# Kernel optimization log

Hardware: AMD Instinct MI355X
Metric: run time of the kernel (lower is better)

The kernel has to match this reference:

```python
import jax, jax.numpy as jnp
import numpy as np

NUM_PERSISTENT = 16
ALIBI_ALPHA = 1.0
START_I = 0
DILATION = 1
LN_EPS = 1e-5


def setup_inputs() -> dict:
    key = jax.random.key(0)
    ks = jax.random.split(key, 16)
    B, S, C, H = 8, 1024, 512, 8
    D = C // H
    P = NUM_PERSISTENT
    Kk = 3
    x = jax.random.normal(ks[0], (B, S, C), dtype=jnp.float32)
    mask = jnp.ones((B, 1, S, S), dtype=jnp.int32)
    sc = 0.02
    Wq = jax.random.normal(ks[1], (D, D), jnp.float32) * sc
    Wk = jax.random.normal(ks[2], (D, D), jnp.float32) * sc
    Wv = jax.random.normal(ks[3], (D, D), jnp.float32) * sc
    pk = jax.random.normal(ks[4], (P, H, D), jnp.float32) * sc
    pv = jax.random.normal(ks[5], (P, H, D), jnp.float32) * sc
    th_pre = jax.random.normal(ks[6], (H, H), jnp.float32) * (1.0 / np.sqrt(H))
    th_post = jax.random.normal(ks[7], (H, H), jnp.float32) * (1.0 / np.sqrt(H))
    fc_w = jax.random.normal(ks[8], (C, C), jnp.float32) * sc
    fc_b = jnp.zeros((C,), jnp.float32)
    conv1_w = jax.random.normal(ks[9], (C, C, Kk), jnp.float32) * 0.01
    conv1_b = jnp.zeros((C,), jnp.float32)
    conv2_w = jax.random.normal(ks[10], (C, C, Kk), jnp.float32) * 0.01
    conv2_b = jnp.zeros((C,), jnp.float32)
    ln_g = jnp.ones((C,), jnp.float32)
    ln_b = jnp.zeros((C,), jnp.float32)
    return dict(x=x, mask=mask, Wq=Wq, Wk=Wk, Wv=Wv, pk=pk, pv=pv,
                th_pre=th_pre, th_post=th_post, fc_w=fc_w, fc_b=fc_b,
                conv1_w=conv1_w, conv1_b=conv1_b, conv2_w=conv2_w,
                conv2_b=conv2_b, ln_g=ln_g, ln_b=ln_b)


def _causal_conv(x_nct, w_oik, b_o, dilation):
    # padding (k-1)*d on both sides + chomp right == pad left only
    k = w_oik.shape[-1]
    p = (k - 1) * dilation
    y = jax.lax.conv_general_dilated(
        x_nct, w_oik, window_strides=(1,), padding=[(p, 0)],
        rhs_dilation=(dilation,), dimension_numbers=("NCH", "OIH", "NCH"))
    return y + b_o[None, :, None]


def reference(x, mask, Wq, Wk, Wv, pk, pv, th_pre, th_post, fc_w, fc_b,
              conv1_w, conv1_b, conv2_w, conv2_b, ln_g, ln_b):
    N, S, C = x.shape
    H = th_pre.shape[0]
    D = C // H
    P = pk.shape[0]

    # ---- MultiHeadAttention (eval: dropout = identity) ----
    xh = x.reshape(N, S, H, D)
    q = jnp.einsum("nshd,ed->nshe", xh, Wq)
    k = jnp.einsum("nshd,ed->nshe", xh, Wk)
    v = jnp.einsum("nshd,ed->nshe", xh, Wv)
    # persistent memory tokens appended along key/value length
    k = jnp.concatenate([k, jnp.broadcast_to(pk[None], (N, P, H, D))], axis=1)
    v = jnp.concatenate([v, jnp.broadcast_to(pv[None], (N, P, H, D))], axis=1)

    energy = jnp.einsum("nqhd,nkhd->nhqk", q, k)  # (N,H,S,S+P)

    # ALiBi bias (symmetric |q-k|), zero over persistent keys
    slopes = 2.0 ** (-(ALIBI_ALPHA * (jnp.arange(1, H + 1, dtype=jnp.float32) + START_I)))
    t = jnp.arange(S, dtype=jnp.float32)
    dist = jnp.abs(t[:, None] - t[None, :])  # (S,S)
    bias = -dist[None, None] * slopes[None, :, None, None]  # (1,H,S,S)
    bias = jnp.pad(bias, ((0, 0), (0, 0), (0, 0), (0, P)))
    energy = energy + bias

    # pre-softmax talking heads (1x1 conv over head axis)
    energy = jnp.einsum("hg,ngqk->nhqk", th_pre, energy)

    ext_mask = jnp.pad(mask, ((0, 0), (0, 0), (0, 0), (0, P)), constant_values=1)
    energy = jnp.where(ext_mask == 0, jnp.float32(-1e4), energy)

    attn = jax.nn.softmax(energy / jnp.sqrt(jnp.float32(C)), axis=-1)
    attn = jnp.einsum("hg,ngqk->nhqk", th_post, attn)

    att_out = jnp.einsum("nhql,nlhd->nqhd", attn, v).reshape(N, S, C)
    att_out = att_out @ fc_w.T + fc_b

    x = x + att_out  # residual (dropout1 identity in eval)

    # ---- TemporalBlock (causal dilated convs, no SE since heads>0) ----
    xc = jnp.transpose(x, (0, 2, 1))  # (N,C,S)
    h = jax.nn.relu(_causal_conv(xc, conv1_w, conv1_b, DILATION))
    h = jax.nn.relu(_causal_conv(h, conv2_w, conv2_b, DILATION))
    out = jax.nn.relu(h + xc)  # downsample is None (in==out)

    # mask out invalid frames
    conv_mask = mask[:, 0, :, 0][:, None, :]  # (N,1,S)
    out = jnp.where(conv_mask == 0, 0.0, out)

    y = jnp.transpose(out, (0, 2, 1))  # (N,S,C)
    mu = jnp.mean(y, axis=-1, keepdims=True)
    var = jnp.mean(jnp.square(y - mu), axis=-1, keepdims=True)
    y = (y - mu) * jax.lax.rsqrt(var + LN_EPS) * ln_g + ln_b
    return y
```

## Files before the change

kernel.cpp:

```cpp
#include <hip/hip_runtime.h>
#include <hip/hip_bf16.h>

#define BN 8
#define SS 1024
#define CC 512
#define HH 8
#define DD 64
#define PP 16
#define KT 1040

typedef __hip_bfloat16 bf16;
typedef unsigned char uchar;
typedef unsigned short ushort;
typedef unsigned int uint;
typedef __attribute__((ext_vector_type(8))) short short8;
typedef __attribute__((ext_vector_type(4))) float f32x4;
typedef __attribute__((ext_vector_type(2))) float f32x2;

__device__ __forceinline__ short f2s(float v){ bf16 b = __float2bfloat16(v); return *(short*)&b; }
__device__ __forceinline__ float s2f(short s){ bf16 b; *(short*)&b = s; return __bfloat162float(b); }
__device__ __forceinline__ uchar f2q(float v){
    return (uchar)__builtin_amdgcn_cvt_pk_fp8_f32(v, v, 0, false);
}

#define MFMA16(a,b,c)  __builtin_amdgcn_mfma_f32_16x16x32_bf16(a,b,c,0,0,0)
#define MFMAF8(a,b,c)  __builtin_amdgcn_mfma_f32_16x16x32_fp8_fp8(a,b,c,0,0,0)

__global__ __launch_bounds__(256) void prep_kernel(
    const float* __restrict__ fc_w, const float* __restrict__ c1w,
    const float* __restrict__ c2w, const float* __restrict__ Wq,
    const float* __restrict__ Wk, const float* __restrict__ Wv,
    const float* __restrict__ th_post,
    short* __restrict__ Bfc, uchar* __restrict__ Bc1,
    uchar* __restrict__ Bc2, short* __restrict__ Bqkv)
{
    int i = blockIdx.x*256 + threadIdx.x;
    const int NFC = 512*512, NCV = 512*1536, NQ = 3*64*64;
    if (i < NFC) {
        int c = i >> 9, r = i & 511;
        int g = r >> 6, d = r & 63;
        float s = 0.f;
        #pragma unroll
        for (int h = 0; h < 8; ++h)
            s += fc_w[(size_t)c*512 + h*64 + d] * th_post[h*8 + g];
        Bfc[i] = f2s(s);
        return;
    }
    i -= NFC;
    if (i < NCV) {
        int o = i/1536, r = i%1536, dk = r>>9, ci = r&511;
        Bc1[i] = f2q(c1w[(o*512+ci)*3+dk] * 16.f); return;
    }
    i -= NCV;
    if (i < NCV) {
        int o = i/1536, r = i%1536, dk = r>>9, ci = r&511;
        Bc2[i] = f2q(c2w[(o*512+ci)*3+dk] * 16.f); return;
    }
    i -= NCV;
    if (i < NQ) {
        int w = i >> 12, rest = i & 4095;
        const float* W = (w==0)?Wq:(w==1)?Wk:Wv;
        Bqkv[i] = f2s(W[((rest>>6)&63)*64 + (rest&63)]);
    }
}

__global__ __launch_bounds__(256) void qkv_mfma(
    const float* __restrict__ x, const short* __restrict__ Bqkv,
    uchar* __restrict__ qf, uchar* __restrict__ kf, uchar* __restrict__ vt)
{
    __shared__ short Xs[64*72];
    __shared__ short Ws[192*72];
    const int tid = threadIdx.x;
    const int m0 = blockIdx.x * 64;
    const int h = blockIdx.y;
    const int wave = tid >> 6, lane = tid & 63;
    const int lr = lane & 15, lq = lane >> 4;

    for (int i = tid; i < 1024; i += 256) {
        int r = i >> 4, cg = (i & 15)*4;
        float4 v = *(const float4*)(x + (size_t)(m0+r)*CC + h*64 + cg);
        Xs[r*72+cg+0] = f2s(v.x); Xs[r*72+cg+1] = f2s(v.y);
        Xs[r*72+cg+2] = f2s(v.z); Xs[r*72+cg+3] = f2s(v.w);
    }
    for (int i = tid; i < 3072; i += 256) {
        int r = i >> 4, cg = (i & 15)*4;
        *(short4*)(Ws + r*72 + cg) = *(const short4*)(Bqkv + (size_t)r*64 + cg);
    }
    __syncthreads();

    f32x4 acc[12];
    #pragma unroll
    for (int nt = 0; nt < 12; ++nt) acc[nt] = {0.f,0.f,0.f,0.f};
    #pragma unroll
    for (int ks = 0; ks < 2; ++ks) {
        int ko = ks*32 + lq*8;
        short8 a = *(const short8*)(Xs + (wave*16 + lr)*72 + ko);
        #pragma unroll
        for (int nt = 0; nt < 12; ++nt) {
            short8 b = *(const short8*)(Ws + (nt*16 + lr)*72 + ko);
            acc[nt] = MFMA16(a, b, acc[nt]);
        }
    }
    #pragma unroll
    for (int nt = 0; nt < 12; ++nt) {
        int ep = nt*16 + lr;
        int w = ep >> 6, e = ep & 63;
        #pragma unroll
        for (int reg = 0; reg < 4; ++reg) {
            int m = m0 + wave*16 + lq*4 + reg;
            int n = m >> 10, s = m & 1023;
            float v = acc[nt][reg];
            if (w == 0)      qf[((size_t)(n*HH+h)*SS + s)*DD + e] = f2q(v);
            else if (w == 1) kf[((size_t)(n*HH+h)*KT + s)*DD + e] = f2q(v);
            else             vt[(((size_t)(n*HH+h))*DD + e)*KT + s] = f2q(v);
        }
    }
}

__global__ __launch_bounds__(256) void persist_kernel(
    const float* __restrict__ pk, const float* __restrict__ pv,
    uchar* __restrict__ kf, uchar* __restrict__ vt)
{
    int idx = blockIdx.x*256 + threadIdx.x;
    if (idx >= BN*HH*PP*DD) return;
    int d = idx & 63, p = (idx >> 6) & 15, h = (idx >> 10) & 7, n = idx >> 13;
    size_t src = ((size_t)p*HH + h)*DD + d;
    kf[(((size_t)(n*HH+h))*KT + SS + p)*DD + d] = f2q(pk[src]);
    vt[(((size_t)(n*HH+h))*DD + d)*KT + SS + p] = f2q(pv[src]);
}

__global__ __launch_bounds__(256) void energy_mfma8(
    const uchar* __restrict__ qf, const uchar* __restrict__ kf,
    uchar* __restrict__ E)
{
    __shared__ uchar Qs[64*72];
    __shared__ uchar Ks[64*72];
    const int tid = threadIdx.x;
    const int kt = blockIdx.x;
    const int mt = blockIdx.y;
    const int nh = blockIdx.z;
    const int wave = tid >> 6, lane = tid & 63;
    const int lr = lane & 15, lq = lane >> 4;

    #pragma unroll
    for (int j = 0; j < 2; ++j) {
        int i = tid + j*256;
        int r = i >> 3, c8 = (i & 7)*8;
        *(uint2*)(Qs + r*72 + c8) =
            *(const uint2*)(qf + ((size_t)nh*SS + mt*64 + r)*DD + c8);
        int kcol = kt*64 + r;
        uint2 kv = {0u, 0u};
        if (kcol < KT)
            kv = *(const uint2*)(kf + ((size_t)nh*KT + kcol)*DD + c8);
        *(uint2*)(Ks + r*72 + c8) = kv;
    }
    __syncthreads();

    f32x4 acc[4];
    #pragma unroll
    for (int nt = 0; nt < 4; ++nt) acc[nt] = {0.f,0.f,0.f,0.f};
    #pragma unroll
    for (int ks = 0; ks < 2; ++ks) {
        int ko = ks*32 + lq*8;
        long a = *(const long*)(Qs + (wave*16 + lr)*72 + ko);
        #pragma unroll
        for (int nt = 0; nt < 4; ++nt) {
            long b = *(const long*)(Ks + (nt*16 + lr)*72 + ko);
            acc[nt] = MFMAF8(a, b, acc[nt]);
        }
    }
    const int n = nh >> 3, h = nh & 7;
    #pragma unroll
    for (int nt = 0; nt < 4; ++nt) {
        int kcol = kt*64 + nt*16 + lr;
        if (kcol >= KT) continue;
        #pragma unroll
        for (int reg = 0; reg < 4; ++reg) {
            int q = mt*64 + wave*16 + lq*4 + reg;
            E[(((size_t)(n*SS + q))*HH + h)*KT + kcol] = f2q(acc[nt][reg]);
        }
    }
}

__global__ __launch_bounds__(256) void softmax_kernel(
    uchar* __restrict__ E, const int* __restrict__ mask,
    const float* __restrict__ th_pre)
{
    __shared__ float thp[64];
    __shared__ float wred[4][8];
    const int tid = threadIdx.x;
    const int wave = tid >> 6, lane = tid & 63;
    const int blk = blockIdx.x;
    const int n = blk >> 10, q = blk & 1023;
    const float invs = 0.044194173824159216f;
    const float l2e  = 1.4426950408889634f;
    if (tid < 64) thp[tid] = th_pre[tid]*(invs*l2e);
    __syncthreads();
    uchar* Eb = E + (size_t)blk*HH*KT;

    const float sl[8] = {0.5f,0.25f,0.125f,0.0625f,
                         0.03125f,0.015625f,0.0078125f,0.00390625f};
    const int* mrow = mask + (size_t)n*SS*SS + (size_t)q*SS;

    const int k0 = tid*4;
    const int4 mk = *(const int4*)(mrow + k0);
    f32x4 dist;
    dist.x = fabsf((float)(q - k0));
    dist.y = fabsf((float)(q - k0 - 1));
    dist.z = fabsf((float)(q - k0 - 2));
    dist.w = fabsf((float)(q - k0 - 3));

    f32x4 tp[8];
    float tl[8];
    float sm[8];
    #pragma unroll
    for (int g = 0; g < 8; ++g) { sm[g] = 0.f; tl[g] = 0.f; }

    {
        f32x4 a[8];
        #pragma unroll
        for (int g = 0; g < 8; ++g) {
            uint u = *(const uint*)(Eb + g*KT + k0);
            f32x2 lo = __builtin_amdgcn_cvt_pk_f32_fp8((int)u, false);
            f32x2 hi = __builtin_amdgcn_cvt_pk_f32_fp8((int)u, true);
            f32x4 r; r.x = lo.x; r.y = lo.y; r.z = hi.x; r.w = hi.y;
            a[g] = r - dist*sl[g];
        }
        #pragma unroll
        for (int h = 0; h < 8; ++h) {
            f32x4 t = {0.f,0.f,0.f,0.f};
            #pragma unroll
            for (int g = 0; g < 8; ++g)
                t += a[g] * thp[h*8 + g];
            f32x4 e;
            e.x = (mk.x == 0) ? 0.f : exp2f(t.x);
            e.y = (mk.y == 0) ? 0.f : exp2f(t.y);
            e.z = (mk.z == 0) ? 0.f : exp2f(t.z);
            e.w = (mk.w == 0) ? 0.f : exp2f(t.w);
            tp[h] = e;
            sm[h] += e.x + e.y + e.z + e.w;
        }
    }
    if (tid < 16) {
        const int k = 1024 + tid;
        float a[8];
        #pragma unroll
        for (int g = 0; g < 8; ++g) {
            f32x2 r = __builtin_amdgcn_cvt_pk_f32_fp8((int)Eb[g*KT + k], false);
            a[g] = r.x;
        }
        #pragma unroll
        for (int h = 0; h < 8; ++h) {
            float t = 0.f;
            #pragma unroll
            for (int g = 0; g < 8; ++g) t = fmaf(thp[h*8 + g], a[g], t);
            float e = exp2f(t);
            tl[h] = e;
            sm[h] += e;
        }
    }
    #pragma unroll
    for (int g = 0; g < 8; ++g) {
        #pragma unroll
        for (int off = 32; off > 0; off >>= 1)
            sm[g] += __shfl_xor(sm[g], off);
    }
    if (lane == 0) {
        #pragma unroll
        for (int g = 0; g < 8; ++g) wred[wave][g] = sm[g];
    }
    __syncthreads();
    float lred[8];
    #pragma unroll
    for (int g = 0; g < 8; ++g)
        lred[g] = 1.0f / (wred[0][g] + wred[1][g] + wred[2][g] + wred[3][g]);

    #pragma unroll
    for (int h = 0; h < 8; ++h) {
        f32x4 e = tp[h] * lred[h];
        int p = __builtin_amdgcn_cvt_pk_fp8_f32(e.x, e.y, 0, false);
        p = __builtin_amdgcn_cvt_pk_fp8_f32(e.z, e.w, p, true);
        *(uint*)(Eb + h*KT + k0) = (uint)p;
    }
    if (tid < 16) {
        const int k = 1024 + tid;
        #pragma unroll
        for (int g = 0; g < 8; ++g)
            Eb[g*KT + k] = f2q(tl[g] * lred[g]);
    }
}

__device__ __forceinline__ void pv_loadP(const uchar* __restrict__ E,
    int n, int h, int ql0, int kt, int tid, uint2* rp)
{
    int r = tid >> 3, cg = (tid & 7)*8;
    int k = kt*64 + cg;
    uint2 v = {0u, 0u};
    if (k < KT)
        v = *(const uint2*)(E + (((size_t)(n*SS + ql0 + r))*HH + h)*KT + k);
    rp[0] = v;
}
__device__ __forceinline__ void pv_loadV(const uchar* __restrict__ vt,
    int nh, int kt, int tid, uint2* rv)
{
    #pragma unroll
    for (int j = 0; j < 2; ++j) {
        int i = tid + j*256;
        int r = i >> 3, cg = (i & 7)*8;
        int k = kt*64 + cg;
        uint2 v = {0u, 0u};
        if (k < KT)
            v = *(const uint2*)(vt + ((size_t)nh*DD + r)*KT + k);
        rv[j] = v;
    }
}

__global__ __launch_bounds__(256) void pv_mfma(
    const uchar* __restrict__ E, const uchar* __restrict__ vt,
    short* __restrict__ AO)
{
    __shared__ uchar Ps[32*72];
    __shared__ uchar Vs[64*72];
    const int tid = threadIdx.x;
    const int ql0 = blockIdx.x * 32;
    const int nh = blockIdx.y;
    const int n = nh >> 3, h = nh & 7;
    const int wave = tid >> 6, lane = tid & 63;
    const int lr = lane & 15, lq = lane >> 4;
    const int mh = wave & 1, nb = (wave >> 1)*32;

    uint2 rp[1], rv[2];
    pv_loadP(E, n, h, ql0, 0, tid, rp);
    pv_loadV(vt, nh, 0, tid, rv);

    f32x4 acc[2];
    acc[0] = {0.f,0.f,0.f,0.f}; acc[1] = {0.f,0.f,0.f,0.f};

    for (int kt = 0; kt < 17; ++kt) {
        if (kt) __syncthreads();
        {
            int r = tid >> 3, cg = (tid & 7)*8;
            *(uint2*)(Ps + r*72 + cg) = rp[0];
        }
        #pragma unroll
        for (int j = 0; j < 2; ++j) {
            int i = tid + j*256;
            *(uint2*)(Vs + (i >> 3)*72 + (i & 7)*8) = rv[j];
        }
        __syncthreads();
        if (kt + 1 < 17) {
            pv_loadP(E, n, h, ql0, kt+1, tid, rp);
            pv_loadV(vt, nh, kt+1, tid, rv);
        }
        #pragma unroll
        for (int ks = 0; ks < 2; ++ks) {
            int ko = ks*32 + lq*8;
            long a = *(const long*)(Ps + (mh*16 + lr)*72 + ko);
            #pragma unroll
            for (int nt = 0; nt < 2; ++nt) {
                long b = *(const long*)(Vs + (nb + nt*16 + lr)*72 + ko);
                acc[nt] = MFMAF8(a, b, acc[nt]);
            }
        }
    }
    #pragma unroll
    for (int nt = 0; nt < 2; ++nt) {
        int d = nb + nt*16 + lr;
        #pragma unroll
        for (int reg = 0; reg < 4; ++reg) {
            int qg = ql0 + mh*16 + lq*4 + reg;
            AO[((size_t)(n*SS) + qg)*CC + h*64 + d] = f2s(acc[nt][reg]);
        }
    }
}

__device__ __forceinline__ void g_load4(const short* __restrict__ src,
    size_t rowstride, int row0, int col0, int tid, short4* r)
{
    #pragma unroll
    for (int j = 0; j < 4; ++j) {
        int i = tid + j*256;
        int rr = i >> 4, cg = (i & 15)*4;
        r[j] = *(const short4*)(src + (size_t)(row0 + rr)*rowstride + col0 + cg);
    }
}
__device__ __forceinline__ void lds_store4(short* __restrict__ dst,
    int tid, const short4* r)
{
    #pragma unroll
    for (int j = 0; j < 4; ++j) {
        int i = tid + j*256;
        *(short4*)(dst + (i >> 4)*72 + (i & 15)*4) = r[j];
    }
}

__global__ __launch_bounds__(256) void fc_mfma(
    const short* __restrict__ A, const short* __restrict__ Bt,
    const float* __restrict__ bias, const float* __restrict__ x,
    short* __restrict__ out, uchar* __restrict__ out8)
{
    __shared__ short As[64*72];
    __shared__ short Bs[64*72];
    const int tid = threadIdx.x;
    const int lin = blockIdx.x + 8*blockIdx.y;
    const int xcd = lin & 7, slot = lin >> 3;
    const int m0 = (xcd*16 + (slot & 15))*64;
    const int n0 = (slot >> 4)*64;
    const int wave = tid >> 6, lane = tid & 63;
    const int lr = lane & 15, lq = lane >> 4;

    short4 ra[4], rb[4];
    g_load4(A, CC, m0, 0, tid, ra);
    g_load4(Bt, CC, n0, 0, tid, rb);

    f32x4 acc[4];
    #pragma unroll
    for (int nt = 0; nt < 4; ++nt) acc[nt] = {0.f,0.f,0.f,0.f};

    for (int kt = 0; kt < CC; kt += 64) {
        if (kt) __syncthreads();
        lds_store4(As, tid, ra);
        lds_store4(Bs, tid, rb);
        __syncthreads();
        if (kt + 64 < CC) {
            g_load4(A, CC, m0, kt+64, tid, ra);
            g_load4(Bt, CC, n0, kt+64, tid, rb);
        }
        #pragma unroll
        for (int ks = 0; ks < 2; ++ks) {
            int ko = ks*32 + lq*8;
            short8 a = *(const short8*)(As + (wave*16 + lr)*72 + ko);
            #pragma unroll
            for (int nt = 0; nt < 4; ++nt) {
                short8 b = *(const short8*)(Bs + (nt*16 + lr)*72 + ko);
                acc[nt] = MFMA16(a, b, acc[nt]);
            }
        }
    }
    #pragma unroll
    for (int nt = 0; nt < 4; ++nt) {
        int nn = n0 + nt*16 + lr;
        #pragma unroll
        for (int reg = 0; reg < 4; ++reg) {
            int m = m0 + wave*16 + lq*4 + reg;
            float v = acc[nt][reg] + bias[nn] + x[(size_t)m*CC + nn];
            out[(size_t)m*CC + nn]  = f2s(v);
            out8[(size_t)m*CC + nn] = f2q(v);
        }
    }
}

__device__ __forceinline__ void conv_loadA8(const uchar* __restrict__ A,
    int m0, int kt, int tid, uint2* ra)
{
    const int shift = (kt >> 9) - 2;
    const int ci0 = kt & 511;
    #pragma unroll
    for (int j = 0; j < 2; ++j) {
        int i = tid + j*256;
        int rr = i >> 3, c8 = (i & 7)*8;
        int m = m0 + rr;
        int s = m & (SS-1);
        uint2 v = {0u, 0u};
        if (s + shift >= 0)
            v = *(const uint2*)(A + (size_t)(m + shift)*CC + ci0 + c8);
        ra[j] = v;
    }
}
__device__ __forceinline__ void g_load8(const uchar* __restrict__ src,
    size_t rowstride, int row0, int col0, int tid, uint2* r)
{
    #pragma unroll
    for (int j = 0; j < 2; ++j) {
        int i = tid + j*256;
        int rr = i >> 3, c8 = (i & 7)*8;
        r[j] = *(const uint2*)(src + (size_t)(row0 + rr)*rowstride + col0 + c8);
    }
}
__device__ __forceinline__ void lds_store8(uchar* __restrict__ dst,
    int tid, const uint2* r)
{
    #pragma unroll
    for (int j = 0; j < 2; ++j) {
        int i = tid + j*256;
        *(uint2*)(dst + (i >> 3)*72 + (i & 7)*8) = r[j];
    }
}

__global__ __launch_bounds__(256) void conv_mfma8(
    const uchar* __restrict__ A, const uchar* __restrict__ Bt,
    const float* __restrict__ bias, uchar* __restrict__ out8,
    short* __restrict__ out16, int f8out)
{
    __shared__ uchar As[64*72];
    __shared__ uchar Bs[64*72];
    const int tid = threadIdx.x;
    const int lin = blockIdx.x + 8*blockIdx.y;
    const int xcd = lin & 7, slot = lin >> 3;
    const int m0 = (xcd*16 + (slot & 15))*64;
    const int n0 = (slot >> 4)*64;
    const int wave = tid >> 6, lane = tid & 63;
    const int lr = lane & 15, lq = lane >> 4;

    uint2 ra[2], rb[2];
    conv_loadA8(A, m0, 0, tid, ra);
    g_load8(Bt, 1536, n0, 0, tid, rb);

    f32x4 acc[4];
    #pragma unroll
    for (int nt = 0; nt < 4; ++nt) acc[nt] = {0.f,0.f,0.f,0.f};

    for (int kt = 0; kt < 1536; kt += 64) {
        if (kt) __syncthreads();
        lds_store8(As, tid, ra);
        lds_store8(Bs, tid, rb);
        __syncthreads();
        if (kt + 64 < 1536) {
            conv_loadA8(A, m0, kt+64, tid, ra);
            g_load8(Bt, 1536, n0, kt+64, tid, rb);
        }
        #pragma unroll
        for (int ks = 0; ks < 2; ++ks) {
            int ko = ks*32 + lq*8;
            long a = *(const long*)(As + (wave*16 + lr)*72 + ko);
            #pragma unroll
            for (int nt = 0; nt < 4; ++nt) {
                long b = *(const long*)(Bs + (nt*16 + lr)*72 + ko);
                acc[nt] = MFMAF8(a, b, acc[nt]);
            }
        }
    }
    #pragma unroll
    for (int nt = 0; nt < 4; ++nt) {
        int nn = n0 + nt*16 + lr;
        #pragma unroll
        for (int reg = 0; reg < 4; ++reg) {
            int m = m0 + wave*16 + lq*4 + reg;
            float v = fmaxf(acc[nt][reg]*0.0625f + bias[nn], 0.f);
            if (f8out) out8[(size_t)m*CC + nn]  = f2q(v);
            else       out16[(size_t)m*CC + nn] = f2s(v);
        }
    }
}

__global__ __launch_bounds__(256) void final_kernel(
    const short* __restrict__ c2, const short* __restrict__ xres,
    const int* __restrict__ mask, const float* __restrict__ g,
    const float* __restrict__ b, float* __restrict__ out)
{
    __shared__ float red[256];
    const int tid = threadIdx.x;
    const int m = blockIdx.x;
    const int n = m >> 10, s = m & 1023;
    const int mk = mask[(size_t)n*SS*SS + (size_t)s*SS];
    const int c0 = tid*2;

    short2 ca = *(const short2*)(c2 + (size_t)m*CC + c0);
    short2 xa = *(const short2*)(xres + (size_t)m*CC + c0);
    float v0 = fmaxf(s2f(ca.x) + s2f(xa.x), 0.f);
    float v1 = fmaxf(s2f(ca.y) + s2f(xa.y), 0.f);
    if (mk == 0) { v0 = 0.f; v1 = 0.f; }

    red[tid] = v0 + v1;
    __syncthreads();
    for (int off = 128; off > 0; off >>= 1) {
        if (tid < off) red[tid] += red[tid + off];
        __syncthreads();
    }
    float mu = red[0] * (1.0f/512.0f);
    __syncthreads();
    float d0 = v0 - mu, d1 = v1 - mu;
    red[tid] = d0*d0 + d1*d1;
    __syncthreads();
    for (int off = 128; off > 0; off >>= 1) {
        if (tid < off) red[tid] += red[tid + off];
        __syncthreads();
    }
    float rstd = rsqrtf(red[0] * (1.0f/512.0f) + 1e-5f);
    float2 gg = *(const float2*)(g + c0);
    float2 bb = *(const float2*)(b + c0);
    float2 o;
    o.x = d0*rstd*gg.x + bb.x;
    o.y = d1*rstd*gg.y + bb.y;
    *(float2*)(out + (size_t)m*CC + c0) = o;
}

extern "C" void kernel_launch(void* const* d_in, const int* in_sizes, int n_in,
                              void* d_out, int out_size, void* d_ws, size_t ws_size,
                              hipStream_t stream)
{
    const float* x      = (const float*)d_in[0];
    const int*   mask   = (const int*)  d_in[1];
    const float* Wq     = (const float*)d_in[2];
    const float* Wk     = (const float*)d_in[3];
    const float* Wv     = (const float*)d_in[4];
    const float* pk     = (const float*)d_in[5];
    const float* pv     = (const float*)d_in[6];
    const float* th_pre = (const float*)d_in[7];
    const float* th_post= (const float*)d_in[8];
    const float* fc_w   = (const float*)d_in[9];
    const float* fc_b   = (const float*)d_in[10];
    const float* c1w    = (const float*)d_in[11];
    const float* c1b    = (const float*)d_in[12];
    const float* c2w    = (const float*)d_in[13];
    const float* c2b    = (const float*)d_in[14];
    const float* lng    = (const float*)d_in[15];
    const float* lnb    = (const float*)d_in[16];
    float* out = (float*)d_out;
    (void)in_sizes; (void)n_in; (void)out_size; (void)ws_size;

    char* ws = (char*)d_ws;
    const size_t SZ_Q  = (size_t)BN*HH*SS*DD;
    const size_t SZ_K  = (size_t)BN*HH*KT*DD;
    const size_t SZ_VT = (size_t)BN*HH*DD*KT;
    const size_t SZ_E  = (size_t)BN*SS*HH*KT;
    const size_t SZ_A  = (size_t)BN*SS*CC*2;
    const size_t SZ_A8 = (size_t)BN*SS*CC;

    uchar* qf  = (uchar*)(ws);
    uchar* kf  = (uchar*)(ws + SZ_Q);
    uchar* vt  = (uchar*)(ws + SZ_Q + SZ_K);
    uchar* E   = (uchar*)(ws + SZ_Q + SZ_K + SZ_VT);
    short* AO  = (short*)(ws + SZ_Q + SZ_K + SZ_VT + SZ_E);
    char*  wend = ws + SZ_Q + SZ_K + SZ_VT + SZ_E + SZ_A;
    short* Bfc = (short*)(wend);
    uchar* Bc1 = (uchar*)(wend + 512*512*2);
    uchar* Bc2 = (uchar*)(wend + 512*512*2 + 512*1536);
    short* Bqkv= (short*)(wend + 512*512*2 + 2*512*1536);
    uchar* xres8 = (uchar*)(wend + 512*512*2 + 2*512*1536 + 3*64*64*2);
    short* c2buf = (short*)(wend + 512*512*2 + 2*512*1536 + 3*64*64*2 + SZ_A8);
    short* xres = (short*)(ws);
    uchar* h18  = (uchar*)E;

    {
        int total = 512*512 + 2*512*1536 + 3*64*64;
        prep_kernel<<<(total + 255)/256, 256, 0, stream>>>(
            fc_w, c1w, c2w, Wq, Wk, Wv, th_post, Bfc, Bc1, Bc2, Bqkv);
    }
    qkv_mfma<<<dim3(BN*SS/64, HH), 256, 0, stream>>>(x, Bqkv, qf, kf, vt);
    persist_kernel<<<(BN*HH*PP*DD + 255)/256, 256, 0, stream>>>(pk, pv, kf, vt);

    energy_mfma8<<<dim3(17, SS/64, BN*HH), 256, 0, stream>>>(qf, kf, E);
    softmax_kernel<<<BN*SS, 256, 0, stream>>>(E, mask, th_pre);
    pv_mfma<<<dim3(SS/32, BN*HH), 256, 0, stream>>>(E, vt, AO);

    fc_mfma<<<dim3(8, 128), 256, 0, stream>>>(AO, Bfc, fc_b, x, xres, xres8);
    conv_mfma8<<<dim3(8, 128), 256, 0, stream>>>(xres8, Bc1, c1b, h18, (short*)nullptr, 1);
    conv_mfma8<<<dim3(8, 128), 256, 0, stream>>>(h18, Bc2, c2b, (uchar*)nullptr, c2buf, 0);
    final_kernel<<<BN*SS, 256, 0, stream>>>(c2buf, xres, mask, lng, lnb, out);
}
```

Before: 309.1 us.

## Loop energy kernel over K tiles with register prefetch; fold ALiBi into softmax

The energy kernel now keeps each Q tile in shared memory and loops over all 17 K tiles inside one block. The next K tile is prefetched into registers while the current tile is being computed, and the grid shrinks from 17x16x64 to 16x64 blocks. The softmax kernel folds the ALiBi distance term through the head-mixing matrix into one per-head coefficient, which removes 8 multiplies per element, and masking is skipped when no element in the group is dead. Fewer blocks lower occupancy and parallelism, and the per-tile loop adds syncthreads overhead.

```diff
diff --git a/kernel.cpp b/kernel.cpp
--- a/kernel.cpp
+++ b/kernel.cpp
@@ -129,6 +129,21 @@
     vt[(((size_t)(n*HH+h))*DD + d)*KT + SS + p] = f2q(pv[src]);
 }
 
+__device__ __forceinline__ void en_loadK(const uchar* __restrict__ kf,
+    int nh, int kt, int tid, uint2* rk)
+{
+    #pragma unroll
+    for (int j = 0; j < 2; ++j) {
+        int i = tid + j*256;
+        int r = i >> 3, c8 = (i & 7)*8;
+        int kcol = kt*64 + r;
+        uint2 v = {0u, 0u};
+        if (kcol < KT)
+            v = *(const uint2*)(kf + ((size_t)nh*KT + kcol)*DD + c8);
+        rk[j] = v;
+    }
+}
+
 __global__ __launch_bounds__(256) void energy_mfma8(
     const uchar* __restrict__ qf, const uchar* __restrict__ kf,
     uchar* __restrict__ E)
@@ -136,11 +151,11 @@
     __shared__ uchar Qs[64*72];
     __shared__ uchar Ks[64*72];
     const int tid = threadIdx.x;
-    const int kt = blockIdx.x;
-    const int mt = blockIdx.y;
-    const int nh = blockIdx.z;
+    const int mt = blockIdx.x;
+    const int nh = blockIdx.y;
     const int wave = tid >> 6, lane = tid & 63;
     const int lr = lane & 15, lq = lane >> 4;
+    const int n = nh >> 3, h = nh & 7;
 
     #pragma unroll
     for (int j = 0; j < 2; ++j) {
@@ -148,36 +163,43 @@
         int r = i >> 3, c8 = (i & 7)*8;
         *(uint2*)(Qs + r*72 + c8) =
             *(const uint2*)(qf + ((size_t)nh*SS + mt*64 + r)*DD + c8);
-        int kcol = kt*64 + r;
-        uint2 kv = {0u, 0u};
-        if (kcol < KT)
-            kv = *(const uint2*)(kf + ((size_t)nh*KT + kcol)*DD + c8);
-        *(uint2*)(Ks + r*72 + c8) = kv;
-    }
-    __syncthreads();
-
-    f32x4 acc[4];
-    #pragma unroll
-    for (int nt = 0; nt < 4; ++nt) acc[nt] = {0.f,0.f,0.f,0.f};
-    #pragma unroll
-    for (int ks = 0; ks < 2; ++ks) {
-        int ko = ks*32 + lq*8;
-        long a = *(const long*)(Qs + (wave*16 + lr)*72 + ko);
+    }
+
+    uint2 rk[2];
+    en_loadK(kf, nh, 0, tid, rk);
+
+    for (int kt = 0; kt < 17; ++kt) {
+        if (kt) __syncthreads();
+        #pragma unroll
+        for (int j = 0; j < 2; ++j) {
+            int i = tid + j*256;
+            *(uint2*)(Ks + (i >> 3)*72 + (i & 7)*8) = rk[j];
+        }
+        __syncthreads();
+        if (kt + 1 < 17) en_loadK(kf, nh, kt+1, tid, rk);
+
+        f32x4 acc[4];
+        #pragma unroll
+        for (int nt = 0; nt < 4; ++nt) acc[nt] = {0.f,0.f,0.f,0.f};
+        #pragma unroll
+        for (int ks = 0; ks < 2; ++ks) {
+            int ko = ks*32 + lq*8;
+            long a = *(const long*)(Qs + (wave*16 + lr)*72 + ko);
+            #pragma unroll
+            for (int nt = 0; nt < 4; ++nt) {
+                long b = *(const long*)(Ks + (nt*16 + lr)*72 + ko);
+                acc[nt] = MFMAF8(a, b, acc[nt]);
+            }
+        }
         #pragma unroll
         for (int nt = 0; nt < 4; ++nt) {
-            long b = *(const long*)(Ks + (nt*16 + lr)*72 + ko);
-            acc[nt] = MFMAF8(a, b, acc[nt]);
-        }
-    }
-    const int n = nh >> 3, h = nh & 7;
-    #pragma unroll
-    for (int nt = 0; nt < 4; ++nt) {
-        int kcol = kt*64 + nt*16 + lr;
-        if (kcol >= KT) continue;
-        #pragma unroll
-        for (int reg = 0; reg < 4; ++reg) {
-            int q = mt*64 + wave*16 + lq*4 + reg;
-            E[(((size_t)(n*SS + q))*HH + h)*KT + kcol] = f2q(acc[nt][reg]);
+            int kcol = kt*64 + nt*16 + lr;
+            if (kcol >= KT) continue;
+            #pragma unroll
+            for (int reg = 0; reg < 4; ++reg) {
+                int q = mt*64 + wave*16 + lq*4 + reg;
+                E[(((size_t)(n*SS + q))*HH + h)*KT + kcol] = f2q(acc[nt][reg]);
+            }
         }
     }
 }
@@ -187,6 +209,7 @@
     const float* __restrict__ th_pre)
 {
     __shared__ float thp[64];
+    __shared__ float ch[8];
     __shared__ float wred[4][8];
     const int tid = threadIdx.x;
     const int wave = tid >> 6, lane = tid & 63;
@@ -195,15 +218,21 @@
     const float invs = 0.044194173824159216f;
     const float l2e  = 1.4426950408889634f;
     if (tid < 64) thp[tid] = th_pre[tid]*(invs*l2e);
+    if (tid < 8) {
+        const float sl[8] = {0.5f,0.25f,0.125f,0.0625f,
+                             0.03125f,0.015625f,0.0078125f,0.00390625f};
+        float c = 0.f;
+        #pragma unroll
+        for (int g = 0; g < 8; ++g) c += th_pre[tid*8+g]*sl[g];
+        ch[tid] = c * (invs*l2e);
+    }
     __syncthreads();
     uchar* Eb = E + (size_t)blk*HH*KT;
-
-    const float sl[8] = {0.5f,0.25f,0.125f,0.0625f,
-                         0.03125f,0.015625f,0.0078125f,0.00390625f};
     const int* mrow = mask + (size_t)n*SS*SS + (size_t)q*SS;
 
     const int k0 = tid*4;
     const int4 mk = *(const int4*)(mrow + k0);
+    const bool anyDead = (mk.x == 0) || (mk.y == 0) || (mk.z == 0) || (mk.w == 0);
     f32x4 dist;
     dist.x = fabsf((float)(q - k0));
     dist.y = fabsf((float)(q - k0 - 1));
@@ -224,7 +253,7 @@
             f32x2 lo = __builtin_amdgcn_cvt_pk_f32_fp8((int)u, false);
             f32x2 hi = __builtin_amdgcn_cvt_pk_f32_fp8((int)u, true);
             f32x4 r; r.x = lo.x; r.y = lo.y; r.z = hi.x; r.w = hi.y;
-            a[g] = r - dist*sl[g];
+            a[g] = r;
         }
         #pragma unroll
         for (int h = 0; h < 8; ++h) {
@@ -232,11 +261,18 @@
             #pragma unroll
             for (int g = 0; g < 8; ++g)
                 t += a[g] * thp[h*8 + g];
+            t -= dist * ch[h];
             f32x4 e;
-            e.x = (mk.x == 0) ? 0.f : exp2f(t.x);
-            e.y = (mk.y == 0) ? 0.f : exp2f(t.y);
-            e.z = (mk.z == 0) ? 0.f : exp2f(t.z);
-            e.w = (mk.w == 0) ? 0.f : exp2f(t.w);
+            e.x = exp2f(t.x);
+            e.y = exp2f(t.y);
+            e.z = exp2f(t.z);
+            e.w = exp2f(t.w);
+            if (anyDead) {
+                if (mk.x == 0) e.x = 0.f;
+                if (mk.y == 0) e.y = 0.f;
+                if (mk.z == 0) e.z = 0.f;
+                if (mk.w == 0) e.w = 0.f;
+            }
             tp[h] = e;
             sm[h] += e.x + e.y + e.z + e.w;
         }
@@ -640,7 +676,7 @@
     qkv_mfma<<<dim3(BN*SS/64, HH), 256, 0, stream>>>(x, Bqkv, qf, kf, vt);
     persist_kernel<<<(BN*HH*PP*DD + 255)/256, 256, 0, stream>>>(pk, pv, kf, vt);
 
-    energy_mfma8<<<dim3(17, SS/64, BN*HH), 256, 0, stream>>>(qf, kf, E);
+    energy_mfma8<<<dim3(SS/64, BN*HH), 256, 0, stream>>>(qf, kf, E);
     softmax_kernel<<<BN*SS, 256, 0, stream>>>(E, mask, th_pre);
     pv_mfma<<<dim3(SS/32, BN*HH), 256, 0, stream>>>(E, vt, AO);
 
```

After: 305.4 us. No clear change (-1.2%).
